# Optimization experiments

Measured on AMD Instinct MI355X. Metric: run time of the kernel, lower is better.

Reference implementation:

```python
import jax, jax.numpy as jnp
import numpy as np

B, S, E, H, HD, RD, MP = 2, 2048, 1024, 16, 64, 32, 8  # batch, seq, embed, heads, head_dim, rotary_dim, mp_num


def rotate_every_two(x):
    # x: [..., D] -> interleave (-x_odd, x_even)
    x1 = x[..., ::2]
    x2 = x[..., 1::2]
    return jnp.stack((-x2, x1), axis=-1).reshape(x.shape)


def apply_rotary(x, sin, cos):
    # x: [B,S,H,RD]; sin/cos: [S, RD//2] -> repeat_interleave(2) -> [1,S,1,RD]
    sin = jnp.repeat(sin, 2, axis=-1)[None, :, None, :]
    cos = jnp.repeat(cos, 2, axis=-1)[None, :, None, :]
    return x * cos + rotate_every_two(x) * sin


def setup_inputs() -> dict:
    key = jax.random.key(0)
    k1, k2, k3 = jax.random.split(key, 3)
    return {
        "hidden_states": jax.random.normal(k1, (B, S, E), dtype=jnp.float32),
        "w_qkv": jax.random.normal(k2, (3 * E, E), dtype=jnp.float32) * 0.02,
        "w_out": jax.random.normal(k3, (E, E), dtype=jnp.float32) * 0.02,
    }


def reference(hidden_states, w_qkv, w_out):
    qkv = hidden_states @ w_qkv.T                      # [B,S,3E]
    local = HD * H // MP                               # 128
    qkv = qkv.reshape(B, S, MP, 3 * local)
    # torch.split order in source is (query, value, key)
    q, v, k = jnp.split(qkv, 3, axis=-1)               # each [B,S,MP,local]

    def split_heads(x):
        return x.reshape(B, S, MP, H // MP, HD).reshape(B, S, H, HD)

    q, k, v = split_heads(q), split_heads(k), split_heads(v)  # [B,S,H,HD]

    # fixed sinusoidal rotary embedding over first RD dims
    inv_freq = 1.0 / 10000 ** (jnp.arange(0, RD, 2, dtype=jnp.float32) / RD)
    sinusoid = jnp.arange(S, dtype=jnp.float32)[:, None] * inv_freq[None, :]  # [S, RD//2]
    sin, cos = jnp.sin(sinusoid), jnp.cos(sinusoid)

    q = jnp.concatenate([apply_rotary(q[..., :RD], sin, cos), q[..., RD:]], axis=-1)
    k = jnp.concatenate([apply_rotary(k[..., :RD], sin, cos), k[..., RD:]], axis=-1)

    # [B,H,S,HD]
    q = q.transpose(0, 2, 1, 3)
    k = k.transpose(0, 2, 1, 3)
    v = v.transpose(0, 2, 1, 3)

    scores = jnp.einsum('bhqd,bhkd->bhqk', q, k) / np.float32(np.sqrt(HD))
    causal = jnp.tril(jnp.ones((S, S), dtype=bool))
    scores = jnp.where(causal[None, None], scores, jnp.float32(-1e9))
    attn = jax.nn.softmax(scores.astype(jnp.float32), axis=-1).astype(q.dtype)
    out = jnp.einsum('bhqk,bhkd->bhqd', attn, v)       # [B,H,S,HD]
    out = out.transpose(0, 2, 1, 3).reshape(B, S, E)
    return out @ w_out.T
```

## Files before the change

kernel.cpp:

```cpp
#include <hip/hip_runtime.h>
#include <hip/hip_bf16.h>

typedef __attribute__((ext_vector_type(8))) short short8;
typedef __attribute__((ext_vector_type(4))) float v4f;

#define ASYNC_COPY16(ldsptr, gptr)                                                        \
  __builtin_amdgcn_global_load_lds((const __attribute__((address_space(1))) void*)(gptr), \
                                   (__attribute__((address_space(3))) void*)(ldsptr),     \
                                   16, 0, 0)

__device__ __forceinline__ unsigned short f2bf(float f) {
  unsigned int u = __float_as_uint(f);
  u += 0x7fffu + ((u >> 16) & 1u);
  return (unsigned short)(u >> 16);
}

__global__ void convert_all(const float* __restrict__ h, const float* __restrict__ wq,
                            const float* __restrict__ wo, unsigned short* __restrict__ ho,
                            unsigned short* __restrict__ wqo, unsigned short* __restrict__ woo) {
  int i = (blockIdx.x * blockDim.x + threadIdx.x) * 4;
  const float* src;
  unsigned short* dst;
  int j;
  if (i < 4194304) { src = h; dst = ho; j = i; }
  else if (i < 7340032) { src = wq; dst = wqo; j = i - 4194304; }
  else { src = wo; dst = woo; j = i - 7340032; }
  float4 v = *(const float4*)(src + j);
  ushort4 o;
  o.x = f2bf(v.x); o.y = f2bf(v.y); o.z = f2bf(v.z); o.w = f2bf(v.w);
  *(ushort4*)(dst + j) = o;
}

#define STAGE_SWZ(tt) ((((tt) & 3) ^ (((tt) >> 3) & 3)) * 8)
#define READ_SWZ(kb, lr) (((kb) ^ (((lr) >> 1) & 3)) * 8)

__global__ __launch_bounds__(256, 6) void gemm_out(const unsigned short* __restrict__ A,
                                                   const unsigned short* __restrict__ Bm,
                                                   float* __restrict__ C, int M, int N, int K) {
  __shared__ __attribute__((aligned(16))) unsigned short As[64 * 32];
  __shared__ __attribute__((aligned(16))) unsigned short Bs[64 * 32];
  int t = threadIdx.x;
  int w = t >> 6, lane = t & 63, kb = lane >> 4, lr = lane & 15;
  int m0 = blockIdx.y * 64, n0 = blockIdx.x * 64;
  int wm = (w >> 1) * 32, wn = (w & 1) * 32;
  v4f acc[2][2];
#pragma unroll
  for (int i = 0; i < 2; i++)
#pragma unroll
    for (int j = 0; j < 2; j++) acc[i][j] = (v4f){0.f, 0.f, 0.f, 0.f};
  int ra = m0 + (t >> 2);
  int rb = n0 + (t >> 2);
  int ca = STAGE_SWZ(t);
  int rs = READ_SWZ(kb, lr);
  for (int k0 = 0; k0 < K; k0 += 32) {
    ASYNC_COPY16(&As[t * 8], A + (size_t)ra * K + k0 + ca);
    ASYNC_COPY16(&Bs[t * 8], Bm + (size_t)rb * K + k0 + ca);
    __syncthreads();
    short8 av[2], bv[2];
#pragma unroll
    for (int i = 0; i < 2; i++) av[i] = *(const short8*)&As[(wm + i * 16 + lr) * 32 + rs];
#pragma unroll
    for (int j = 0; j < 2; j++) bv[j] = *(const short8*)&Bs[(wn + j * 16 + lr) * 32 + rs];
#pragma unroll
    for (int i = 0; i < 2; i++)
#pragma unroll
      for (int j = 0; j < 2; j++)
        acc[i][j] = __builtin_amdgcn_mfma_f32_16x16x32_bf16(av[i], bv[j], acc[i][j], 0, 0, 0);
    __syncthreads();
  }
#pragma unroll
  for (int i = 0; i < 2; i++) {
    int row = m0 + wm + i * 16 + kb * 4;
#pragma unroll
    for (int j = 0; j < 2; j++) {
      int col = n0 + wn + j * 16 + lr;
#pragma unroll
      for (int r = 0; r < 4; r++) C[(size_t)(row + r) * N + col] = acc[i][j][r];
    }
  }
}

__global__ __launch_bounds__(256, 6) void gemm_qkv(const unsigned short* __restrict__ A,
                                                   const unsigned short* __restrict__ Bm,
                                                   unsigned short* __restrict__ Q,
                                                   unsigned short* __restrict__ Ko,
                                                   unsigned short* __restrict__ Vt) {
  constexpr int Kd = 1024;
  __shared__ __attribute__((aligned(16))) unsigned short As[128 * 32];
  __shared__ __attribute__((aligned(16))) unsigned short Bs[64 * 32];
  int t = threadIdx.x;
  int w = t >> 6, lane = t & 63, kb = lane >> 4, lr = lane & 15;
  int m0 = blockIdx.y * 128, n0 = blockIdx.x * 64;
  int wm = (w >> 1) * 64, wn = (w & 1) * 32;
  v4f acc[4][2];
#pragma unroll
  for (int i = 0; i < 4; i++)
#pragma unroll
    for (int j = 0; j < 2; j++) acc[i][j] = (v4f){0.f, 0.f, 0.f, 0.f};
  int ra = m0 + (t >> 2);
  int rb = n0 + (t >> 2);
  int ca = STAGE_SWZ(t);
  int rs = READ_SWZ(kb, lr);
  for (int k0 = 0; k0 < Kd; k0 += 32) {
    ASYNC_COPY16(&As[t * 8],        A + (size_t)ra * Kd + k0 + ca);
    ASYNC_COPY16(&As[2048 + t * 8], A + (size_t)(ra + 64) * Kd + k0 + ca);
    ASYNC_COPY16(&Bs[t * 8],        Bm + (size_t)rb * Kd + k0 + ca);
    __syncthreads();
    short8 av[4], bv[2];
#pragma unroll
    for (int i = 0; i < 4; i++) av[i] = *(const short8*)&As[(wm + i * 16 + lr) * 32 + rs];
#pragma unroll
    for (int j = 0; j < 2; j++) bv[j] = *(const short8*)&Bs[(wn + j * 16 + lr) * 32 + rs];
#pragma unroll
    for (int i = 0; i < 4; i++)
#pragma unroll
      for (int j = 0; j < 2; j++)
        acc[i][j] = __builtin_amdgcn_mfma_f32_16x16x32_bf16(av[i], bv[j], acc[i][j], 0, 0, 0);
    __syncthreads();
  }
  int X = n0 >> 6;
  int mp = X / 6;
  int sub = X - mp * 6;
  int type = sub >> 1;
  int ii = sub & 1;
  int h = mp * 2 + ii;
  const float qs = 0.125f * 1.4426950408889634f;
  if (type == 1) {
#pragma unroll
    for (int i = 0; i < 4; i++) {
      int row = m0 + wm + i * 16 + kb * 4;
#pragma unroll
      for (int j = 0; j < 2; j++) {
        int dim = wn + j * 16 + lr;
#pragma unroll
        for (int r = 0; r < 4; r++) {
          int m = row + r;
          int b = m >> 11, sl = m & 2047;
          int bh = b * 16 + h;
          int p = (sl & ~31) | ((sl & 15) << 1) | ((sl >> 4) & 1);
          Vt[(size_t)bh * 131072 + (size_t)dim * 2048 + p] = f2bf(acc[i][j][r]);
        }
      }
    }
  } else {
    unsigned short* dst = (type == 0) ? Q : Ko;
    float scale = (type == 0) ? qs : 1.0f;
#pragma unroll
    for (int i = 0; i < 4; i++) {
      int row = m0 + wm + i * 16 + kb * 4;
#pragma unroll
      for (int j = 0; j < 2; j++) {
        int dim = wn + j * 16 + lr;
        float vals[4];
#pragma unroll
        for (int r = 0; r < 4; r++) vals[r] = acc[i][j][r];
        if (dim < 32) {
          int jp = dim >> 1;
          float invf = expf(-(float)jp * 0.57564627324851142f);
#pragma unroll
          for (int r = 0; r < 4; r++) {
            int sl = (row + r) & 2047;
            float ang = (float)sl * invf;
            float sn, cs;
            sincosf(ang, &sn, &cs);
            float partner = __shfl_xor(vals[r], 1);
            float self = vals[r] * cs;
            vals[r] = (lr & 1) ? fmaf(partner, sn, self) : fmaf(-partner, sn, self);
          }
        }
#pragma unroll
        for (int r = 0; r < 4; r++) {
          int m = row + r;
          int b = m >> 11, sl = m & 2047;
          int bh = b * 16 + h;
          dst[(((size_t)(bh * 2048 + sl)) << 6) + dim] = f2bf(vals[r] * scale);
        }
      }
    }
  }
}

__global__ __launch_bounds__(256, 6) void attn_fused(const unsigned short* __restrict__ Qg,
                                                     const unsigned short* __restrict__ Kg,
                                                     const unsigned short* __restrict__ Vtg,
                                                     unsigned short* __restrict__ AO) {
  __shared__ __attribute__((aligned(16))) unsigned short Ks[2 * 2048];
  __shared__ __attribute__((aligned(16))) unsigned short Vs[2 * 2048];
  __shared__ __attribute__((aligned(16))) unsigned short Ps[4 * 16 * 40];
  int t = threadIdx.x;
  int w = t >> 6, lane = t & 63, kb = lane >> 4, lr = lane & 15;
  int gid = blockIdx.x;
  int g3 = gid & 7;
  int b2 = (gid >> 3) & 3;
  int z = (gid >> 5) & 7;
  int quarter = gid >> 8;
  int bh = g3 * 4 + b2;
  int qtile = (quarter == 0) ? z : (quarter == 1) ? (31 - z) : (quarter == 2) ? (z + 8) : (23 - z);
  int m0 = qtile * 64;
  const unsigned short* Qb = Qg + (size_t)bh * 2048 * 64;
  const unsigned short* Kb = Kg + (size_t)bh * 2048 * 64;
  const unsigned short* Vb = Vtg + (size_t)bh * 64 * 2048;

  short8 aq0 = *(const short8*)(Qb + (size_t)(m0 + w * 16 + lr) * 64 + kb * 8);
  short8 aq1 = *(const short8*)(Qb + (size_t)(m0 + w * 16 + lr) * 64 + 32 + kb * 8);

  v4f acc[4];
  float lp[4];
#pragma unroll
  for (int n = 0; n < 4; n++) acc[n] = (v4f){0.f, 0.f, 0.f, 0.f};
#pragma unroll
  for (int r = 0; r < 4; r++) lp[r] = 0.f;

  int nkt = 2 * qtile + 2;
  int mrow = w * 16 + kb * 4;

  int kc = t >> 5, krow_s = t & 31;
  int vc = t >> 6, vd = t & 63;
  auto stage = [&](int kt, int buf) {
    int base = buf * 2048;
    ASYNC_COPY16(&Ks[base + t * 8], Kb + (size_t)(kt * 32 + krow_s) * 64 + kc * 8);
    ASYNC_COPY16(&Vs[base + t * 8], Vb + (size_t)vd * 2048 + kt * 32 + vc * 8);
  };

  stage(0, 0);
  __syncthreads();

  unsigned short* Pw = &Ps[w * 640];
  for (int kt = 0; kt < nkt; kt++) {
    int cur = (kt & 1) * 2048;
    if (kt + 1 < nkt) stage(kt + 1, (kt + 1) & 1);
    v4f sc[2];
#pragma unroll
    for (int n2 = 0; n2 < 2; n2++) {
      int krow = n2 * 16 + lr;
      short8 bk0 = *(const short8*)&Ks[cur + (kb * 32 + krow) * 8];
      short8 bk1 = *(const short8*)&Ks[cur + ((kb + 4) * 32 + krow) * 8];
      v4f zz = (v4f){0.f, 0.f, 0.f, 0.f};
      zz = __builtin_amdgcn_mfma_f32_16x16x32_bf16(aq0, bk0, zz, 0, 0, 0);
      zz = __builtin_amdgcn_mfma_f32_16x16x32_bf16(aq1, bk1, zz, 0, 0, 0);
      sc[n2] = zz;
    }
    if (kt >= 2 * qtile) {
#pragma unroll
      for (int n2 = 0; n2 < 2; n2++)
#pragma unroll
        for (int r = 0; r < 4; r++) {
          int key = kt * 32 + n2 * 16 + lr;
          if (key > m0 + mrow + r) sc[n2][r] = -1e30f;
        }
    }
#pragma unroll
    for (int r = 0; r < 4; r++) {
      float p0 = exp2f(sc[0][r]);
      float p1 = exp2f(sc[1][r]);
      lp[r] += p0 + p1;
      __hip_bfloat162 pb = __float22bfloat162_rn(float2{p0, p1});
      *(__hip_bfloat162*)&Pw[(mrow & 15) * 40 + r * 40 + lr * 2] = pb;
    }
    short8 ap = *(const short8*)&Pw[lr * 40 + kb * 8];
#pragma unroll
    for (int dt = 0; dt < 4; dt++) {
      int d = dt * 16 + lr;
      short8 bv = *(const short8*)&Vs[cur + (kb * 64 + d) * 8];
      acc[dt] = __builtin_amdgcn_mfma_f32_16x16x32_bf16(ap, bv, acc[dt], 0, 0, 0);
    }
    __syncthreads();
  }
  int b = bh >> 4, h = bh & 15;
#pragma unroll
  for (int r = 0; r < 4; r++) {
    float s = lp[r];
#pragma unroll
    for (int off = 1; off < 16; off <<= 1) s += __shfl_xor(s, off);
    float inv = 1.0f / s;
    int qrow = m0 + mrow + r;
#pragma unroll
    for (int dt = 0; dt < 4; dt++)
      AO[(size_t)(b * 2048 + qrow) * 1024 + h * 64 + dt * 16 + lr] = f2bf(acc[dt][r] * inv);
  }
}

extern "C" void kernel_launch(void* const* d_in, const int* in_sizes, int n_in,
                              void* d_out, int out_size, void* d_ws, size_t ws_size,
                              hipStream_t stream) {
  const float* hidden = (const float*)d_in[0];
  const float* w_qkv = (const float*)d_in[1];
  const float* w_out = (const float*)d_in[2];
  float* out = (float*)d_out;
  char* ws = (char*)d_ws;
  unsigned short* hid_bf = (unsigned short*)(ws);
  unsigned short* wqkv_bf = (unsigned short*)(ws + (8ull << 20));
  unsigned short* wout_bf = (unsigned short*)(ws + (14ull << 20));
  unsigned short* Qb = (unsigned short*)(ws + (16ull << 20));
  unsigned short* Kb = (unsigned short*)(ws + (24ull << 20));
  unsigned short* Vt = (unsigned short*)(ws + (32ull << 20));
  unsigned short* AO = (unsigned short*)(ws + (40ull << 20));

  convert_all<<<8192, 256, 0, stream>>>(hidden, w_qkv, w_out, hid_bf, wqkv_bf, wout_bf);
  gemm_qkv<<<dim3(48, 32), 256, 0, stream>>>(hid_bf, wqkv_bf, Qb, Kb, Vt);
  attn_fused<<<1024, 256, 0, stream>>>(Qb, Kb, Vt, AO);
  gemm_out<<<dim3(16, 64), 256, 0, stream>>>(AO, wout_bf, out, 4096, 1024, 1024);
}
```

Baseline: 201.9 us.

## Split long causal query tiles across two key ranges with combine pass

Query tiles in the upper half of the sequence are split into two blocks covering separate key ranges, writing unnormalized fp32 partial outputs and row sums; a new combine kernel adds them and normalizes into the bf16 attention output. This raises block count and shortens the longest blocks to reduce load imbalance and tail latency. It adds an extra launch and fp32 partial traffic through global memory.

```diff
diff --git a/kernel.cpp b/kernel.cpp
--- a/kernel.cpp
+++ b/kernel.cpp
@@ -183,7 +183,9 @@
 __global__ __launch_bounds__(256, 6) void attn_fused(const unsigned short* __restrict__ Qg,
                                                      const unsigned short* __restrict__ Kg,
                                                      const unsigned short* __restrict__ Vtg,
-                                                     unsigned short* __restrict__ AO) {
+                                                     unsigned short* __restrict__ AO,
+                                                     float* __restrict__ PO,
+                                                     float* __restrict__ PL) {
   __shared__ __attribute__((aligned(16))) unsigned short Ks[2 * 2048];
   __shared__ __attribute__((aligned(16))) unsigned short Vs[2 * 2048];
   __shared__ __attribute__((aligned(16))) unsigned short Ps[4 * 16 * 40];
@@ -193,9 +195,18 @@
   int g3 = gid & 7;
   int b2 = (gid >> 3) & 3;
   int z = (gid >> 5) & 7;
-  int quarter = gid >> 8;
+  int coset = gid >> 8;
   int bh = g3 * 4 + b2;
-  int qtile = (quarter == 0) ? z : (quarter == 1) ? (31 - z) : (quarter == 2) ? (z + 8) : (23 - z);
+  int j = (coset == 0) ? (2 * z)
+        : (coset == 1) ? (15 - 2 * z)
+        : (coset == 2) ? (16 + z)
+        : (coset == 3) ? (31 - z)
+        : (coset == 4) ? (32 + z)
+                       : (47 - z);
+  int qtile, kt0, kt1, mode;
+  if (j < 16)      { qtile = j;      mode = 0; kt0 = 0;          kt1 = 2 * qtile + 2; }
+  else if (j < 32) { qtile = j;      mode = 1; kt0 = 0;          kt1 = qtile + 1; }
+  else             { qtile = j - 16; mode = 2; kt0 = qtile + 1;  kt1 = 2 * qtile + 2; }
   int m0 = qtile * 64;
   const unsigned short* Qb = Qg + (size_t)bh * 2048 * 64;
   const unsigned short* Kb = Kg + (size_t)bh * 2048 * 64;
@@ -211,7 +222,6 @@
 #pragma unroll
   for (int r = 0; r < 4; r++) lp[r] = 0.f;
 
-  int nkt = 2 * qtile + 2;
   int mrow = w * 16 + kb * 4;
 
   int kc = t >> 5, krow_s = t & 31;
@@ -222,13 +232,15 @@
     ASYNC_COPY16(&Vs[base + t * 8], Vb + (size_t)vd * 2048 + kt * 32 + vc * 8);
   };
 
-  stage(0, 0);
+  stage(kt0, 0);
   __syncthreads();
 
   unsigned short* Pw = &Ps[w * 640];
-  for (int kt = 0; kt < nkt; kt++) {
-    int cur = (kt & 1) * 2048;
-    if (kt + 1 < nkt) stage(kt + 1, (kt + 1) & 1);
+  int niter = kt1 - kt0;
+  for (int it = 0; it < niter; it++) {
+    int kt = kt0 + it;
+    int cur = (it & 1) * 2048;
+    if (it + 1 < niter) stage(kt + 1, (it + 1) & 1);
     v4f sc[2];
 #pragma unroll
     for (int n2 = 0; n2 < 2; n2++) {
@@ -266,18 +278,58 @@
     }
     __syncthreads();
   }
+  float s[4];
+#pragma unroll
+  for (int r = 0; r < 4; r++) {
+    s[r] = lp[r];
+#pragma unroll
+    for (int off = 1; off < 16; off <<= 1) s[r] += __shfl_xor(s[r], off);
+  }
+  if (mode == 0) {
+    int b = bh >> 4, h = bh & 15;
+#pragma unroll
+    for (int r = 0; r < 4; r++) {
+      float inv = 1.0f / s[r];
+      int qrow = m0 + mrow + r;
+#pragma unroll
+      for (int dt = 0; dt < 4; dt++)
+        AO[(size_t)(b * 2048 + qrow) * 1024 + h * 64 + dt * 16 + lr] = f2bf(acc[dt][r] * inv);
+    }
+  } else {
+    int hf = mode - 1;
+    size_t pbase = ((size_t)hf * 512 + bh * 16 + (qtile - 16)) * 4096;
+    size_t plbase = (size_t)hf * 32768 + (bh * 16 + (qtile - 16)) * 64;
+#pragma unroll
+    for (int r = 0; r < 4; r++) {
+      if (lr == 0) PL[plbase + mrow + r] = s[r];
+#pragma unroll
+      for (int dt = 0; dt < 4; dt++)
+        PO[pbase + (size_t)(mrow + r) * 64 + dt * 16 + lr] = acc[dt][r];
+    }
+  }
+}
+
+__global__ __launch_bounds__(256) void combine(const float* __restrict__ PO,
+                                               const float* __restrict__ PL,
+                                               unsigned short* __restrict__ AO) {
+  int idx = blockIdx.x * 256 + threadIdx.x;
+  int d4 = (idx & 15) * 4;
+  int row10 = (idx >> 4) & 1023;
+  int bh = idx >> 14;
+  int q16 = row10 >> 6, lrow = row10 & 63;
+  size_t pbase = (((size_t)(bh * 16 + q16)) * 64 + lrow) * 64 + d4;
+  float4 a = *(const float4*)&PO[pbase];
+  float4 c = *(const float4*)&PO[2097152 + pbase];
+  float l = PL[(bh * 16 + q16) * 64 + lrow] + PL[32768 + (bh * 16 + q16) * 64 + lrow];
+  float inv = 1.0f / l;
+  ushort4 o;
+  o.x = f2bf((a.x + c.x) * inv);
+  o.y = f2bf((a.y + c.y) * inv);
+  o.z = f2bf((a.z + c.z) * inv);
+  o.w = f2bf((a.w + c.w) * inv);
   int b = bh >> 4, h = bh & 15;
-#pragma unroll
-  for (int r = 0; r < 4; r++) {
-    float s = lp[r];
-#pragma unroll
-    for (int off = 1; off < 16; off <<= 1) s += __shfl_xor(s, off);
-    float inv = 1.0f / s;
-    int qrow = m0 + mrow + r;
-#pragma unroll
-    for (int dt = 0; dt < 4; dt++)
-      AO[(size_t)(b * 2048 + qrow) * 1024 + h * 64 + dt * 16 + lr] = f2bf(acc[dt][r] * inv);
-  }
+  int qrow = 1024 + row10;
+  *(ushort4*)&AO[(size_t)(b * 2048 + qrow) * 1024 + h * 64 + d4] = o;
 }
 
 extern "C" void kernel_launch(void* const* d_in, const int* in_sizes, int n_in,
@@ -295,9 +347,12 @@
   unsigned short* Kb = (unsigned short*)(ws + (24ull << 20));
   unsigned short* Vt = (unsigned short*)(ws + (32ull << 20));
   unsigned short* AO = (unsigned short*)(ws + (40ull << 20));
+  float* PO = (float*)(ws + (48ull << 20));
+  float* PL = (float*)(ws + (64ull << 20));
 
   convert_all<<<8192, 256, 0, stream>>>(hidden, w_qkv, w_out, hid_bf, wqkv_bf, wout_bf);
   gemm_qkv<<<dim3(48, 32), 256, 0, stream>>>(hid_bf, wqkv_bf, Qb, Kb, Vt);
-  attn_fused<<<1024, 256, 0, stream>>>(Qb, Kb, Vt, AO);
+  attn_fused<<<1536, 256, 0, stream>>>(Qb, Kb, Vt, AO, PO, PL);
+  combine<<<2048, 256, 0, stream>>>(PO, PL, AO);
   gemm_out<<<dim3(16, 64), 256, 0, stream>>>(AO, wout_bf, out, 4096, 1024, 1024);
 }
```

After: 192.9 us. -4.5%, faster.
